# Kernel tuning notes

Measured on AMD Instinct MI355X. Metric: run time of the kernel, lower is better.

The kernel has to match this reference:

```python
import jax, jax.numpy as jnp
import numpy as np

B, N, C, D = 4, 4096, 1024, 32  # batch, tokens, channels, head dim
EPS = 1e-15
PAD_VAL = 1.0


def setup_inputs() -> dict:
    key = jax.random.key(0)
    k1, k2, k3 = jax.random.split(key, 3)
    x = jax.random.normal(k1, (B, N, C), dtype=jnp.float32)
    W_qkv = jax.random.normal(k2, (3 * C, C), dtype=jnp.float32) * 0.02
    W_proj = jax.random.normal(k3, (C, C), dtype=jnp.float32) * 0.02
    b_proj = jnp.zeros((C,), dtype=jnp.float32)
    return {"x": x, "W_qkv": W_qkv, "W_proj": W_proj, "b_proj": b_proj}


def reference(x, W_qkv, W_proj, b_proj):
    Bx, Nx, Cx = x.shape
    h = Cx // D
    # qkv projection (no bias), then split as torch: reshape(B,N,3,C).permute(0,2,3,1)
    qkv = jnp.einsum('bnc,oc->bno', x, W_qkv)            # [B,N,3C]
    qkv = qkv.reshape(Bx, Nx, 3, Cx).transpose(0, 2, 3, 1)  # [B,3,C,N]
    q, k, v = qkv[:, 0], qkv[:, 1], qkv[:, 2]
    q = jax.nn.relu(q.reshape(Bx, h, D, Nx))             # [B,h,D,N]
    k = jax.nn.relu(k.reshape(Bx, h, D, Nx)).transpose(0, 1, 3, 2)  # [B,h,N,D]
    v = v.reshape(Bx, h, D, Nx)                          # [B,h,D,N]
    # pad v with a row of PAD_VAL=1 to carry the normalizer
    v = jnp.concatenate([v, jnp.full((Bx, h, 1, Nx), PAD_VAL, v.dtype)], axis=2)  # [B,h,D+1,N]
    vk = jnp.einsum('bhdn,bhne->bhde', v, k)             # [B,h,D+1,D]
    out = jnp.einsum('bhde,bhen->bhdn', vk, q)           # [B,h,D+1,N]
    out = out[:, :, :-1] / (out[:, :, -1:] + EPS)        # [B,h,D,N]
    out = out.reshape(Bx, Cx, Nx).transpose(0, 2, 1)     # [B,N,C]
    return jnp.einsum('bnc,oc->bno', out, W_proj) + b_proj
```

## Files before the change

kernel.cpp:

```cpp
#include <hip/hip_runtime.h>


using us8   = __attribute__((ext_vector_type(8))) unsigned short;
using us4   = __attribute__((ext_vector_type(4))) unsigned short;
using s8v   = __attribute__((ext_vector_type(8))) short;
using f32x4 = __attribute__((ext_vector_type(4))) float;

__device__ __forceinline__ unsigned short f2bf(float f) {
    union { float f; unsigned int u; } c; c.f = f;
    unsigned int r = c.u + 0x7fffu + ((c.u >> 16) & 1u);
    return (unsigned short)(r >> 16);
}
__device__ __forceinline__ float bf2f(unsigned short u) {
    union { unsigned int u; float f; } c; c.u = ((unsigned int)u) << 16;
    return c.f;
}

__device__ __forceinline__ void async16(const unsigned short* g, unsigned short* l) {
    __builtin_amdgcn_global_load_lds(
        (const __attribute__((address_space(1))) unsigned int*)g,
        (__attribute__((address_space(3))) unsigned int*)l, 16, 0, 0);
}

__global__ __launch_bounds__(256)
void prep(const float* __restrict__ x, const float* __restrict__ wq,
          const float* __restrict__ wp, unsigned short* __restrict__ xb,
          unsigned short* __restrict__ wqb, unsigned short* __restrict__ wpb,
          float* __restrict__ vkws) {
    const int NX = 16777216 / 8, NQ = 3145728 / 8, NP = 1048576 / 8, NZ = 135168 / 8;
    int gid = blockIdx.x * 256 + threadIdx.x;
    const float* in; unsigned short* out; int i;
    if (gid < NX)                    { in = x;  out = xb;  i = gid * 8; }
    else if (gid < NX + NQ)          { in = wq; out = wqb; i = (gid - NX) * 8; }
    else if (gid < NX + NQ + NP)     { in = wp; out = wpb; i = (gid - NX - NQ) * 8; }
    else if (gid < NX + NQ + NP + NZ) {
        int z = (gid - NX - NQ - NP) * 8;
        f32x4 zero = {};
        *(f32x4*)(vkws + z) = zero; *(f32x4*)(vkws + z + 4) = zero;
        return;
    } else return;
    float4 a = *(const float4*)(in + i);
    float4 b = *(const float4*)(in + i + 4);
    us8 o;
    o[0] = f2bf(a.x); o[1] = f2bf(a.y); o[2] = f2bf(a.z); o[3] = f2bf(a.w);
    o[4] = f2bf(b.x); o[5] = f2bf(b.y); o[6] = f2bf(b.z); o[7] = f2bf(b.w);
    *(us8*)(out + i) = o;
}

template <int MODE>
__global__ __launch_bounds__(256)
void gemm_bt(const unsigned short* __restrict__ A,
             const unsigned short* __restrict__ Bt,
             void* __restrict__ C, unsigned short* __restrict__ kvT,
             const float* __restrict__ bias,
             int M, int N, int K) {
    __shared__ unsigned short As0[128 * 32], As1[128 * 32];
    __shared__ unsigned short Bs0[128 * 32], Bs1[128 * 32];

    const int tid  = threadIdx.x;
    const int lane = tid & 63;
    const int wv   = tid >> 6;
    const int wr   = wv >> 1, wc = wv & 1;

    const int MT  = M >> 7;
    const int bpg = MT * 8;
    const int g   = blockIdx.x / bpg;
    const int r   = blockIdx.x % bpg;
    const int tM  = (r >> 3) * 128;
    const int tN  = (g * 8 + (r & 7)) * 128;

    f32x4 acc[4][4] = {};

    const int sseg = ((lane & 3) ^ ((lane >> 3) & 3)) * 8;
    const unsigned short* Ag = A + (size_t)(tM + wv * 32 + (lane >> 2)) * K + sseg;
    const unsigned short* Bg = Bt + (size_t)(tN + wv * 32 + (lane >> 2)) * K + sseg;
    const int wo = wv * 32 * 32;

    const int mrow = lane & 15;
    const int kqx  = (((lane >> 4) ^ ((lane >> 1) & 3))) * 8;

    for (int k0 = 0; k0 < K; k0 += 64) {
        __syncthreads();
        async16(Ag + k0,               &As0[wo]);
        async16(Ag + k0 + 16 * K,      &As0[wo + 16 * 32]);
        async16(Ag + k0 + 32,          &As1[wo]);
        async16(Ag + k0 + 32 + 16 * K, &As1[wo + 16 * 32]);
        async16(Bg + k0,               &Bs0[wo]);
        async16(Bg + k0 + 16 * K,      &Bs0[wo + 16 * 32]);
        async16(Bg + k0 + 32,          &Bs1[wo]);
        async16(Bg + k0 + 32 + 16 * K, &Bs1[wo + 16 * 32]);
        asm volatile("s_waitcnt vmcnt(0)" ::: "memory");
        __syncthreads();
        s8v af[4], bf[4];
#pragma unroll
        for (int mi = 0; mi < 4; ++mi)
            af[mi] = *(const s8v*)&As0[(wr * 64 + mi * 16 + mrow) * 32 + kqx];
#pragma unroll
        for (int ni = 0; ni < 4; ++ni)
            bf[ni] = *(const s8v*)&Bs0[(wc * 64 + ni * 16 + mrow) * 32 + kqx];
#pragma unroll
        for (int mi = 0; mi < 4; ++mi)
#pragma unroll
            for (int ni = 0; ni < 4; ++ni)
                acc[mi][ni] = __builtin_amdgcn_mfma_f32_16x16x32_bf16(
                    af[mi], bf[ni], acc[mi][ni], 0, 0, 0);
#pragma unroll
        for (int mi = 0; mi < 4; ++mi)
            af[mi] = *(const s8v*)&As1[(wr * 64 + mi * 16 + mrow) * 32 + kqx];
#pragma unroll
        for (int ni = 0; ni < 4; ++ni)
            bf[ni] = *(const s8v*)&Bs1[(wc * 64 + ni * 16 + mrow) * 32 + kqx];
#pragma unroll
        for (int mi = 0; mi < 4; ++mi)
#pragma unroll
            for (int ni = 0; ni < 4; ++ni)
                acc[mi][ni] = __builtin_amdgcn_mfma_f32_16x16x32_bf16(
                    af[mi], bf[ni], acc[mi][ni], 0, 0, 0);
    }

    const int crow0 = (lane >> 4) * 4;
    const int ccol  = lane & 15;
    if (MODE == 0 && tN >= 1024) {
        const int b2 = tM >> 12;
        const int nb0 = (tM & 4095) + wr * 64;
#pragma unroll
        for (int mi = 0; mi < 4; ++mi) {
            int nbase = nb0 + mi * 16 + crow0;
#pragma unroll
            for (int ni = 0; ni < 4; ++ni) {
                int col = tN + wc * 64 + ni * 16 + ccol;
                f32x4 v = acc[mi][ni];
                if (col < 2048) {
                    v[0] = fmaxf(v[0], 0.f); v[1] = fmaxf(v[1], 0.f);
                    v[2] = fmaxf(v[2], 0.f); v[3] = fmaxf(v[3], 0.f);
                }
                us4 o;
                o[0] = f2bf(v[0]); o[1] = f2bf(v[1]);
                o[2] = f2bf(v[2]); o[3] = f2bf(v[3]);
                *(us4*)&kvT[((size_t)b2 * 2048 + (col - 1024)) * 4096 + nbase] = o;
            }
        }
    } else {
#pragma unroll
        for (int mi = 0; mi < 4; ++mi)
#pragma unroll
            for (int ni = 0; ni < 4; ++ni) {
                int row = tM + wr * 64 + mi * 16 + crow0;
                int col = tN + wc * 64 + ni * 16 + ccol;
#pragma unroll
                for (int r2 = 0; r2 < 4; ++r2) {
                    float v = acc[mi][ni][r2];
                    if (MODE == 0) {
                        v = fmaxf(v, 0.f);
                        ((unsigned short*)C)[(size_t)(row + r2) * 1024 + col] = f2bf(v);
                    } else {
                        ((float*)C)[(size_t)(row + r2) * N + col] = v + bias[col];
                    }
                }
            }
    }
}

__global__ __launch_bounds__(256)
void lite_vk(const unsigned short* __restrict__ kvT, float* __restrict__ vkws) {
    const int bh = blockIdx.x, ck = blockIdx.y;
    const int b = bh >> 5, h = bh & 31;
    const int S = 136;
    __shared__ unsigned short Ks[32 * S];
    __shared__ unsigned short Vs[32 * S];
    __shared__ float Rs[4][1088];
    const int t = threadIdx.x, lane = t & 63, wv = t >> 6;
    const unsigned short* Kp = kvT + ((size_t)b * 2048 + h * 32) * 4096 + ck * 512;
    const unsigned short* Vp = kvT + ((size_t)b * 2048 + 1024 + h * 32) * 4096 + ck * 512;
    const int sr = t >> 3, ss = (t & 7) * 16;
    f32x4 acc00 = {}, acc01 = {}, acc10 = {}, acc11 = {}, accO0 = {}, accO1 = {};
    s8v ones;
#pragma unroll
    for (int j = 0; j < 8; ++j) ones[j] = (short)0x3F80;
    const int mrow = lane & 15, kq = (lane >> 4) * 8;

    for (int tile = 0; tile < 4; ++tile) {
        int go = tile * 128 + ss;
        us8 k0v = *(const us8*)(Kp + (size_t)sr * 4096 + go);
        us8 k1v = *(const us8*)(Kp + (size_t)sr * 4096 + go + 8);
        us8 v0v = *(const us8*)(Vp + (size_t)sr * 4096 + go);
        us8 v1v = *(const us8*)(Vp + (size_t)sr * 4096 + go + 8);
        __syncthreads();
        *(us8*)&Ks[sr * S + ss]     = k0v;
        *(us8*)&Ks[sr * S + ss + 8] = k1v;
        *(us8*)&Vs[sr * S + ss]     = v0v;
        *(us8*)&Vs[sr * S + ss + 8] = v1v;
        __syncthreads();
        int ko = wv * 32 + kq;
        s8v a0 = *(const s8v*)&Vs[(mrow)      * S + ko];
        s8v a1 = *(const s8v*)&Vs[(16 + mrow) * S + ko];
        s8v b0 = *(const s8v*)&Ks[(mrow)      * S + ko];
        s8v b1 = *(const s8v*)&Ks[(16 + mrow) * S + ko];
        acc00 = __builtin_amdgcn_mfma_f32_16x16x32_bf16(a0, b0, acc00, 0, 0, 0);
        acc01 = __builtin_amdgcn_mfma_f32_16x16x32_bf16(a0, b1, acc01, 0, 0, 0);
        acc10 = __builtin_amdgcn_mfma_f32_16x16x32_bf16(a1, b0, acc10, 0, 0, 0);
        acc11 = __builtin_amdgcn_mfma_f32_16x16x32_bf16(a1, b1, acc11, 0, 0, 0);
        accO0 = __builtin_amdgcn_mfma_f32_16x16x32_bf16(ones, b0, accO0, 0, 0, 0);
        accO1 = __builtin_amdgcn_mfma_f32_16x16x32_bf16(ones, b1, accO1, 0, 0, 0);
    }

    const int ccol = lane & 15, crow = (lane >> 4) * 4;
    float* R = Rs[wv];
#pragma unroll
    for (int r2 = 0; r2 < 4; ++r2) {
        R[(crow + r2) * 32 + ccol]           = acc00[r2];
        R[(crow + r2) * 32 + 16 + ccol]      = acc01[r2];
        R[(16 + crow + r2) * 32 + ccol]      = acc10[r2];
        R[(16 + crow + r2) * 32 + 16 + ccol] = acc11[r2];
    }
    if ((lane >> 4) == 0) {
        R[1024 + ccol]      = accO0[0];
        R[1024 + 16 + ccol] = accO1[0];
    }
    __syncthreads();
    float* vkb = vkws + bh * (33 * 32);
    for (int i = t; i < 1056; i += 256) {
        float s = Rs[0][i] + Rs[1][i] + Rs[2][i] + Rs[3][i];
        atomicAdd(&vkb[i], s);
    }
}

__global__ __launch_bounds__(256)
void lite_apply(const unsigned short* __restrict__ qb,
                const float* __restrict__ vkws,
                unsigned short* __restrict__ yb) {
    const int bh = blockIdx.x, nb = blockIdx.y;
    const int b = bh >> 5, h = bh & 31;
    __shared__ unsigned short vkh[48 * 32];
    __shared__ unsigned short vkl[48 * 32];
    const int t = threadIdx.x;
    for (int i = t; i < 48 * 32; i += 256) {
        float v = (i < 33 * 32) ? vkws[bh * (33 * 32) + i] : 0.f;
        unsigned short hi = f2bf(v);
        vkh[i] = hi;
        vkl[i] = f2bf(v - bf2f(hi));
    }
    __syncthreads();

    const int lane = t & 63, wv = t >> 6;
    const int col = lane & 15, quad = lane >> 4;
    s8v b0h = *(const s8v*)&vkh[(col)      * 32 + quad * 8];
    s8v b0l = *(const s8v*)&vkl[(col)      * 32 + quad * 8];
    s8v b1h = *(const s8v*)&vkh[(16 + col) * 32 + quad * 8];
    s8v b1l = *(const s8v*)&vkl[(16 + col) * 32 + quad * 8];
    s8v b2h = *(const s8v*)&vkh[(32 + col) * 32 + quad * 8];
    s8v b2l = *(const s8v*)&vkl[(32 + col) * 32 + quad * 8];

    const int ntile = nb * 256 + wv * 64;
#pragma unroll
    for (int mi = 0; mi < 4; ++mi) {
        int tok = ntile + mi * 16 + col;
        const unsigned short* qp =
            qb + (size_t)(b * 4096 + tok) * 1024 + h * 32 + quad * 8;
        s8v a = *(const s8v*)qp;
        f32x4 n0 = {}, n1 = {}, dd = {};
        n0 = __builtin_amdgcn_mfma_f32_16x16x32_bf16(b0h, a, n0, 0, 0, 0);
        n0 = __builtin_amdgcn_mfma_f32_16x16x32_bf16(b0l, a, n0, 0, 0, 0);
        n1 = __builtin_amdgcn_mfma_f32_16x16x32_bf16(b1h, a, n1, 0, 0, 0);
        n1 = __builtin_amdgcn_mfma_f32_16x16x32_bf16(b1l, a, n1, 0, 0, 0);
        dd = __builtin_amdgcn_mfma_f32_16x16x32_bf16(b2h, a, dd, 0, 0, 0);
        dd = __builtin_amdgcn_mfma_f32_16x16x32_bf16(b2l, a, dd, 0, 0, 0);
        float den  = __shfl(dd[0], col, 64);
        float rinv = 1.f / (den + 1e-15f);
        us4 o0, o1;
#pragma unroll
        for (int r = 0; r < 4; ++r) {
            o0[r] = f2bf(n0[r] * rinv);
            o1[r] = f2bf(n1[r] * rinv);
        }
        size_t o = (size_t)(b * 4096 + tok) * 1024 + h * 32;
        *(us4*)&yb[o + quad * 4]      = o0;
        *(us4*)&yb[o + 16 + quad * 4] = o1;
    }
}

extern "C" void kernel_launch(void* const* d_in, const int* in_sizes, int n_in,
                              void* d_out, int out_size, void* d_ws, size_t ws_size,
                              hipStream_t stream) {
    const float* x     = (const float*)d_in[0];
    const float* Wqkv  = (const float*)d_in[1];
    const float* Wproj = (const float*)d_in[2];
    const float* bproj = (const float*)d_in[3];
    float* out = (float*)d_out;

    const int M = 16384, Cdim = 1024, O1 = 3072;

    unsigned short* xb     = (unsigned short*)d_ws;
    unsigned short* wqkvb  = xb + (size_t)M * Cdim;
    unsigned short* wprojb = wqkvb + (size_t)O1 * Cdim;
    unsigned short* qb     = wprojb + (size_t)Cdim * Cdim;
    unsigned short* kvT    = qb + (size_t)M * Cdim;
    unsigned short* ybuf   = kvT + (size_t)4 * 2048 * 4096;
    float* vkws            = (float*)(ybuf + (size_t)M * Cdim);

    const int PREP_GROUPS = (16777216 + 3145728 + 1048576 + 135168) / 8;
    prep<<<(PREP_GROUPS + 255) / 256, 256, 0, stream>>>(
        x, Wqkv, Wproj, xb, wqkvb, wprojb, vkws);

    gemm_bt<0><<<(M / 128) * (O1 / 128), 256, 0, stream>>>(
        xb, wqkvb, (void*)qb, kvT, nullptr, M, O1, Cdim);

    lite_vk<<<dim3(128, 8), 256, 0, stream>>>(kvT, vkws);
    lite_apply<<<dim3(128, 16), 256, 0, stream>>>(qb, vkws, ybuf);

    gemm_bt<1><<<(M / 128) * (Cdim / 128), 256, 0, stream>>>(
        ybuf, wprojb, (void*)out, nullptr, bproj, M, Cdim, Cdim);
}
```

Baseline: 359.7 us.

## Fuse vk, apply and projection GEMM into one persistent kernel with grid barriers

Merges the lite_vk, lite_apply and output projection GEMM into a single 512-block persistent kernel. The phases are separated by software grid barriers on an atomic counter that prep zeroes. Each block processes several work units per phase. The aim is to remove two kernel launch gaps and tail effects between small kernels. In exchange it adds spin-wait barrier overhead, relies on all 512 blocks being co-resident (deadlock risk otherwise), and gives the projection GEMM a fixed grid of 512 blocks each doing two tiles.

New measurement: 465.5 us. 1.29x slower.

```diff
diff --git a/kernel.cpp b/kernel.cpp
--- a/kernel.cpp
+++ b/kernel.cpp
@@ -20,6 +20,17 @@
     __builtin_amdgcn_global_load_lds(
         (const __attribute__((address_space(1))) unsigned int*)g,
         (__attribute__((address_space(3))) unsigned int*)l, 16, 0, 0);
+}
+
+__device__ __forceinline__ void grid_barrier(unsigned* cnt, unsigned target) {
+    __syncthreads();
+    if (threadIdx.x == 0) {
+        __threadfence();
+        atomicAdd(cnt, 1u);
+        while (atomicAdd(cnt, 0u) < target) {}
+        __threadfence();
+    }
+    __syncthreads();
 }
 
 __global__ __launch_bounds__(256)
@@ -27,7 +38,8 @@
           const float* __restrict__ wp, unsigned short* __restrict__ xb,
           unsigned short* __restrict__ wqb, unsigned short* __restrict__ wpb,
           float* __restrict__ vkws) {
-    const int NX = 16777216 / 8, NQ = 3145728 / 8, NP = 1048576 / 8, NZ = 135168 / 8;
+    const int NX = 16777216 / 8, NQ = 3145728 / 8, NP = 1048576 / 8;
+    const int NZ = (135168 + 16) / 8;
     int gid = blockIdx.x * 256 + threadIdx.x;
     const float* in; unsigned short* out; int i;
     if (gid < NX)                    { in = x;  out = xb;  i = gid * 8; }
@@ -47,13 +59,11 @@
     *(us8*)(out + i) = o;
 }
 
-template <int MODE>
 __global__ __launch_bounds__(256)
-void gemm_bt(const unsigned short* __restrict__ A,
-             const unsigned short* __restrict__ Bt,
-             void* __restrict__ C, unsigned short* __restrict__ kvT,
-             const float* __restrict__ bias,
-             int M, int N, int K) {
+void gemm_qkv(const unsigned short* __restrict__ A,
+              const unsigned short* __restrict__ Bt,
+              unsigned short* __restrict__ Cq, unsigned short* __restrict__ kvT,
+              int M, int N, int K) {
     __shared__ unsigned short As0[128 * 32], As1[128 * 32];
     __shared__ unsigned short Bs0[128 * 32], Bs1[128 * 32];
 
@@ -120,7 +130,7 @@
 
     const int crow0 = (lane >> 4) * 4;
     const int ccol  = lane & 15;
-    if (MODE == 0 && tN >= 1024) {
+    if (tN >= 1024) {
         const int b2 = tM >> 12;
         const int nb0 = (tM & 4095) + wr * 64;
 #pragma unroll
@@ -149,133 +159,214 @@
                 int col = tN + wc * 64 + ni * 16 + ccol;
 #pragma unroll
                 for (int r2 = 0; r2 < 4; ++r2) {
-                    float v = acc[mi][ni][r2];
-                    if (MODE == 0) {
-                        v = fmaxf(v, 0.f);
-                        ((unsigned short*)C)[(size_t)(row + r2) * 1024 + col] = f2bf(v);
-                    } else {
-                        ((float*)C)[(size_t)(row + r2) * N + col] = v + bias[col];
-                    }
+                    float v = fmaxf(acc[mi][ni][r2], 0.f);
+                    Cq[(size_t)(row + r2) * 1024 + col] = f2bf(v);
                 }
             }
     }
 }
 
-__global__ __launch_bounds__(256)
-void lite_vk(const unsigned short* __restrict__ kvT, float* __restrict__ vkws) {
-    const int bh = blockIdx.x, ck = blockIdx.y;
-    const int b = bh >> 5, h = bh & 31;
-    const int S = 136;
-    __shared__ unsigned short Ks[32 * S];
-    __shared__ unsigned short Vs[32 * S];
-    __shared__ float Rs[4][1088];
-    const int t = threadIdx.x, lane = t & 63, wv = t >> 6;
-    const unsigned short* Kp = kvT + ((size_t)b * 2048 + h * 32) * 4096 + ck * 512;
-    const unsigned short* Vp = kvT + ((size_t)b * 2048 + 1024 + h * 32) * 4096 + ck * 512;
-    const int sr = t >> 3, ss = (t & 7) * 16;
-    f32x4 acc00 = {}, acc01 = {}, acc10 = {}, acc11 = {}, accO0 = {}, accO1 = {};
-    s8v ones;
-#pragma unroll
-    for (int j = 0; j < 8; ++j) ones[j] = (short)0x3F80;
-    const int mrow = lane & 15, kq = (lane >> 4) * 8;
-
-    for (int tile = 0; tile < 4; ++tile) {
-        int go = tile * 128 + ss;
-        us8 k0v = *(const us8*)(Kp + (size_t)sr * 4096 + go);
-        us8 k1v = *(const us8*)(Kp + (size_t)sr * 4096 + go + 8);
-        us8 v0v = *(const us8*)(Vp + (size_t)sr * 4096 + go);
-        us8 v1v = *(const us8*)(Vp + (size_t)sr * 4096 + go + 8);
-        __syncthreads();
-        *(us8*)&Ks[sr * S + ss]     = k0v;
-        *(us8*)&Ks[sr * S + ss + 8] = k1v;
-        *(us8*)&Vs[sr * S + ss]     = v0v;
-        *(us8*)&Vs[sr * S + ss + 8] = v1v;
-        __syncthreads();
-        int ko = wv * 32 + kq;
-        s8v a0 = *(const s8v*)&Vs[(mrow)      * S + ko];
-        s8v a1 = *(const s8v*)&Vs[(16 + mrow) * S + ko];
-        s8v b0 = *(const s8v*)&Ks[(mrow)      * S + ko];
-        s8v b1 = *(const s8v*)&Ks[(16 + mrow) * S + ko];
-        acc00 = __builtin_amdgcn_mfma_f32_16x16x32_bf16(a0, b0, acc00, 0, 0, 0);
-        acc01 = __builtin_amdgcn_mfma_f32_16x16x32_bf16(a0, b1, acc01, 0, 0, 0);
-        acc10 = __builtin_amdgcn_mfma_f32_16x16x32_bf16(a1, b0, acc10, 0, 0, 0);
-        acc11 = __builtin_amdgcn_mfma_f32_16x16x32_bf16(a1, b1, acc11, 0, 0, 0);
-        accO0 = __builtin_amdgcn_mfma_f32_16x16x32_bf16(ones, b0, accO0, 0, 0, 0);
-        accO1 = __builtin_amdgcn_mfma_f32_16x16x32_bf16(ones, b1, accO1, 0, 0, 0);
-    }
-
-    const int ccol = lane & 15, crow = (lane >> 4) * 4;
-    float* R = Rs[wv];
-#pragma unroll
-    for (int r2 = 0; r2 < 4; ++r2) {
-        R[(crow + r2) * 32 + ccol]           = acc00[r2];
-        R[(crow + r2) * 32 + 16 + ccol]      = acc01[r2];
-        R[(16 + crow + r2) * 32 + ccol]      = acc10[r2];
-        R[(16 + crow + r2) * 32 + 16 + ccol] = acc11[r2];
-    }
-    if ((lane >> 4) == 0) {
-        R[1024 + ccol]      = accO0[0];
-        R[1024 + 16 + ccol] = accO1[0];
-    }
-    __syncthreads();
-    float* vkb = vkws + bh * (33 * 32);
-    for (int i = t; i < 1056; i += 256) {
-        float s = Rs[0][i] + Rs[1][i] + Rs[2][i] + Rs[3][i];
-        atomicAdd(&vkb[i], s);
-    }
-}
-
-__global__ __launch_bounds__(256)
-void lite_apply(const unsigned short* __restrict__ qb,
-                const float* __restrict__ vkws,
-                unsigned short* __restrict__ yb) {
-    const int bh = blockIdx.x, nb = blockIdx.y;
-    const int b = bh >> 5, h = bh & 31;
-    __shared__ unsigned short vkh[48 * 32];
-    __shared__ unsigned short vkl[48 * 32];
-    const int t = threadIdx.x;
-    for (int i = t; i < 48 * 32; i += 256) {
-        float v = (i < 33 * 32) ? vkws[bh * (33 * 32) + i] : 0.f;
-        unsigned short hi = f2bf(v);
-        vkh[i] = hi;
-        vkl[i] = f2bf(v - bf2f(hi));
-    }
-    __syncthreads();
-
+__global__ __launch_bounds__(256, 2)
+void attn_tail(const unsigned short* __restrict__ kvT,
+               const unsigned short* __restrict__ qb,
+               unsigned short* __restrict__ ybuf,
+               const unsigned short* __restrict__ wprojb,
+               const float* __restrict__ bias,
+               float* __restrict__ out,
+               float* __restrict__ vkws, unsigned* cnt) {
+    __shared__ char lds[34816];
+    const int blk = blockIdx.x, t = threadIdx.x;
     const int lane = t & 63, wv = t >> 6;
-    const int col = lane & 15, quad = lane >> 4;
-    s8v b0h = *(const s8v*)&vkh[(col)      * 32 + quad * 8];
-    s8v b0l = *(const s8v*)&vkl[(col)      * 32 + quad * 8];
-    s8v b1h = *(const s8v*)&vkh[(16 + col) * 32 + quad * 8];
-    s8v b1l = *(const s8v*)&vkl[(16 + col) * 32 + quad * 8];
-    s8v b2h = *(const s8v*)&vkh[(32 + col) * 32 + quad * 8];
-    s8v b2l = *(const s8v*)&vkl[(32 + col) * 32 + quad * 8];
-
-    const int ntile = nb * 256 + wv * 64;
-#pragma unroll
-    for (int mi = 0; mi < 4; ++mi) {
-        int tok = ntile + mi * 16 + col;
-        const unsigned short* qp =
-            qb + (size_t)(b * 4096 + tok) * 1024 + h * 32 + quad * 8;
-        s8v a = *(const s8v*)qp;
-        f32x4 n0 = {}, n1 = {}, dd = {};
-        n0 = __builtin_amdgcn_mfma_f32_16x16x32_bf16(b0h, a, n0, 0, 0, 0);
-        n0 = __builtin_amdgcn_mfma_f32_16x16x32_bf16(b0l, a, n0, 0, 0, 0);
-        n1 = __builtin_amdgcn_mfma_f32_16x16x32_bf16(b1h, a, n1, 0, 0, 0);
-        n1 = __builtin_amdgcn_mfma_f32_16x16x32_bf16(b1l, a, n1, 0, 0, 0);
-        dd = __builtin_amdgcn_mfma_f32_16x16x32_bf16(b2h, a, dd, 0, 0, 0);
-        dd = __builtin_amdgcn_mfma_f32_16x16x32_bf16(b2l, a, dd, 0, 0, 0);
-        float den  = __shfl(dd[0], col, 64);
-        float rinv = 1.f / (den + 1e-15f);
-        us4 o0, o1;
-#pragma unroll
-        for (int r = 0; r < 4; ++r) {
-            o0[r] = f2bf(n0[r] * rinv);
-            o1[r] = f2bf(n1[r] * rinv);
+
+    {
+        const int S = 136;
+        unsigned short* Ks = (unsigned short*)lds;
+        unsigned short* Vs = (unsigned short*)(lds + 8704);
+        float* Rsb = (float*)(lds + 17408);
+        const int sr = t >> 3, ss = (t & 7) * 16;
+        const int mrow = lane & 15, kq = (lane >> 4) * 8;
+        s8v ones;
+#pragma unroll
+        for (int j2 = 0; j2 < 8; ++j2) ones[j2] = (short)0x3F80;
+
+        for (int j = 0; j < 2; ++j) {
+            const int u = blk * 2 + j;
+            const int bh = u >> 3, ck = u & 7;
+            const int b = bh >> 5, h = bh & 31;
+            const unsigned short* Kp = kvT + ((size_t)b * 2048 + h * 32) * 4096 + ck * 512;
+            const unsigned short* Vp = kvT + ((size_t)b * 2048 + 1024 + h * 32) * 4096 + ck * 512;
+            f32x4 a00 = {}, a01 = {}, a10 = {}, a11 = {}, aO0 = {}, aO1 = {};
+            for (int tile = 0; tile < 4; ++tile) {
+                int go = tile * 128 + ss;
+                us8 k0v = *(const us8*)(Kp + (size_t)sr * 4096 + go);
+                us8 k1v = *(const us8*)(Kp + (size_t)sr * 4096 + go + 8);
+                us8 v0v = *(const us8*)(Vp + (size_t)sr * 4096 + go);
+                us8 v1v = *(const us8*)(Vp + (size_t)sr * 4096 + go + 8);
+                __syncthreads();
+                *(us8*)&Ks[sr * S + ss]     = k0v;
+                *(us8*)&Ks[sr * S + ss + 8] = k1v;
+                *(us8*)&Vs[sr * S + ss]     = v0v;
+                *(us8*)&Vs[sr * S + ss + 8] = v1v;
+                __syncthreads();
+                int ko = wv * 32 + kq;
+                s8v a0 = *(const s8v*)&Vs[(mrow)      * S + ko];
+                s8v a1 = *(const s8v*)&Vs[(16 + mrow) * S + ko];
+                s8v b0 = *(const s8v*)&Ks[(mrow)      * S + ko];
+                s8v b1 = *(const s8v*)&Ks[(16 + mrow) * S + ko];
+                a00 = __builtin_amdgcn_mfma_f32_16x16x32_bf16(a0, b0, a00, 0, 0, 0);
+                a01 = __builtin_amdgcn_mfma_f32_16x16x32_bf16(a0, b1, a01, 0, 0, 0);
+                a10 = __builtin_amdgcn_mfma_f32_16x16x32_bf16(a1, b0, a10, 0, 0, 0);
+                a11 = __builtin_amdgcn_mfma_f32_16x16x32_bf16(a1, b1, a11, 0, 0, 0);
+                aO0 = __builtin_amdgcn_mfma_f32_16x16x32_bf16(ones, b0, aO0, 0, 0, 0);
+                aO1 = __builtin_amdgcn_mfma_f32_16x16x32_bf16(ones, b1, aO1, 0, 0, 0);
+            }
+            const int ccol = lane & 15, crow = (lane >> 4) * 4;
+            float* R = Rsb + wv * 1088;
+#pragma unroll
+            for (int r2 = 0; r2 < 4; ++r2) {
+                R[(crow + r2) * 32 + ccol]           = a00[r2];
+                R[(crow + r2) * 32 + 16 + ccol]      = a01[r2];
+                R[(16 + crow + r2) * 32 + ccol]      = a10[r2];
+                R[(16 + crow + r2) * 32 + 16 + ccol] = a11[r2];
+            }
+            if ((lane >> 4) == 0) {
+                R[1024 + ccol]      = aO0[0];
+                R[1024 + 16 + ccol] = aO1[0];
+            }
+            __syncthreads();
+            float* vkb = vkws + bh * (33 * 32);
+            for (int i = t; i < 1056; i += 256) {
+                float s = Rsb[i] + Rsb[1088 + i] + Rsb[2176 + i] + Rsb[3264 + i];
+                atomicAdd(&vkb[i], s);
+            }
+            __syncthreads();
         }
-        size_t o = (size_t)(b * 4096 + tok) * 1024 + h * 32;
-        *(us4*)&yb[o + quad * 4]      = o0;
-        *(us4*)&yb[o + 16 + quad * 4] = o1;
+    }
+    grid_barrier(cnt, 512);
+
+    {
+        unsigned short* vkh = (unsigned short*)lds;
+        unsigned short* vkl = (unsigned short*)(lds + 3072);
+        const int col = lane & 15, quad = lane >> 4;
+        for (int j = 0; j < 4; ++j) {
+            const int u = blk * 4 + j;
+            const int bh = u >> 4, nb = u & 15;
+            const int b = bh >> 5, h = bh & 31;
+            for (int i = t; i < 48 * 32; i += 256) {
+                float v = (i < 33 * 32) ? vkws[bh * (33 * 32) + i] : 0.f;
+                unsigned short hi = f2bf(v);
+                vkh[i] = hi;
+                vkl[i] = f2bf(v - bf2f(hi));
+            }
+            __syncthreads();
+            s8v b0h = *(const s8v*)&vkh[(col)      * 32 + quad * 8];
+            s8v b0l = *(const s8v*)&vkl[(col)      * 32 + quad * 8];
+            s8v b1h = *(const s8v*)&vkh[(16 + col) * 32 + quad * 8];
+            s8v b1l = *(const s8v*)&vkl[(16 + col) * 32 + quad * 8];
+            s8v b2h = *(const s8v*)&vkh[(32 + col) * 32 + quad * 8];
+            s8v b2l = *(const s8v*)&vkl[(32 + col) * 32 + quad * 8];
+            const int ntile = nb * 256 + wv * 64;
+#pragma unroll
+            for (int mi = 0; mi < 4; ++mi) {
+                int tok = ntile + mi * 16 + col;
+                const unsigned short* qp =
+                    qb + (size_t)(b * 4096 + tok) * 1024 + h * 32 + quad * 8;
+                s8v a = *(const s8v*)qp;
+                f32x4 n0 = {}, n1 = {}, dd = {};
+                n0 = __builtin_amdgcn_mfma_f32_16x16x32_bf16(b0h, a, n0, 0, 0, 0);
+                n0 = __builtin_amdgcn_mfma_f32_16x16x32_bf16(b0l, a, n0, 0, 0, 0);
+                n1 = __builtin_amdgcn_mfma_f32_16x16x32_bf16(b1h, a, n1, 0, 0, 0);
+                n1 = __builtin_amdgcn_mfma_f32_16x16x32_bf16(b1l, a, n1, 0, 0, 0);
+                dd = __builtin_amdgcn_mfma_f32_16x16x32_bf16(b2h, a, dd, 0, 0, 0);
+                dd = __builtin_amdgcn_mfma_f32_16x16x32_bf16(b2l, a, dd, 0, 0, 0);
+                float den  = __shfl(dd[0], col, 64);
+                float rinv = 1.f / (den + 1e-15f);
+                us4 o0, o1;
+#pragma unroll
+                for (int r2 = 0; r2 < 4; ++r2) {
+                    o0[r2] = f2bf(n0[r2] * rinv);
+                    o1[r2] = f2bf(n1[r2] * rinv);
+                }
+                size_t o = (size_t)(b * 4096 + tok) * 1024 + h * 32;
+                *(us4*)&ybuf[o + quad * 4]      = o0;
+                *(us4*)&ybuf[o + 16 + quad * 4] = o1;
+            }
+            __syncthreads();
+        }
+    }
+    grid_barrier(cnt, 1024);
+
+    {
+        unsigned short* As0 = (unsigned short*)lds;
+        unsigned short* As1 = (unsigned short*)(lds + 8192);
+        unsigned short* Bs0 = (unsigned short*)(lds + 16384);
+        unsigned short* Bs1 = (unsigned short*)(lds + 24576);
+        const int K = 1024;
+        const int wr = wv >> 1, wc = wv & 1;
+        const int sseg = ((lane & 3) ^ ((lane >> 3) & 3)) * 8;
+        const int mrow = lane & 15;
+        const int kqx  = (((lane >> 4) ^ ((lane >> 1) & 3))) * 8;
+        const int wo = wv * 32 * 32;
+
+        for (int j = 0; j < 2; ++j) {
+            const int u = blk * 2 + j;
+            const int tM = (u >> 3) * 128;
+            const int tN = (u & 7) * 128;
+            f32x4 acc[4][4] = {};
+            const unsigned short* Ag = ybuf + (size_t)(tM + wv * 32 + (lane >> 2)) * K + sseg;
+            const unsigned short* Bg = wprojb + (size_t)(tN + wv * 32 + (lane >> 2)) * K + sseg;
+            for (int k0 = 0; k0 < K; k0 += 64) {
+                __syncthreads();
+                async16(Ag + k0,               &As0[wo]);
+                async16(Ag + k0 + 16 * K,      &As0[wo + 16 * 32]);
+                async16(Ag + k0 + 32,          &As1[wo]);
+                async16(Ag + k0 + 32 + 16 * K, &As1[wo + 16 * 32]);
+                async16(Bg + k0,               &Bs0[wo]);
+                async16(Bg + k0 + 16 * K,      &Bs0[wo + 16 * 32]);
+                async16(Bg + k0 + 32,          &Bs1[wo]);
+                async16(Bg + k0 + 32 + 16 * K, &Bs1[wo + 16 * 32]);
+                asm volatile("s_waitcnt vmcnt(0)" ::: "memory");
+                __syncthreads();
+                s8v af[4], bf[4];
+#pragma unroll
+                for (int mi = 0; mi < 4; ++mi)
+                    af[mi] = *(const s8v*)&As0[(wr * 64 + mi * 16 + mrow) * 32 + kqx];
+#pragma unroll
+                for (int ni = 0; ni < 4; ++ni)
+                    bf[ni] = *(const s8v*)&Bs0[(wc * 64 + ni * 16 + mrow) * 32 + kqx];
+#pragma unroll
+                for (int mi = 0; mi < 4; ++mi)
+#pragma unroll
+                    for (int ni = 0; ni < 4; ++ni)
+                        acc[mi][ni] = __builtin_amdgcn_mfma_f32_16x16x32_bf16(
+                            af[mi], bf[ni], acc[mi][ni], 0, 0, 0);
+#pragma unroll
+                for (int mi = 0; mi < 4; ++mi)
+                    af[mi] = *(const s8v*)&As1[(wr * 64 + mi * 16 + mrow) * 32 + kqx];
+#pragma unroll
+                for (int ni = 0; ni < 4; ++ni)
+                    bf[ni] = *(const s8v*)&Bs1[(wc * 64 + ni * 16 + mrow) * 32 + kqx];
+#pragma unroll
+                for (int mi = 0; mi < 4; ++mi)
+#pragma unroll
+                    for (int ni = 0; ni < 4; ++ni)
+                        acc[mi][ni] = __builtin_amdgcn_mfma_f32_16x16x32_bf16(
+                            af[mi], bf[ni], acc[mi][ni], 0, 0, 0);
+            }
+            const int crow0 = (lane >> 4) * 4;
+            const int ccol  = lane & 15;
+#pragma unroll
+            for (int mi = 0; mi < 4; ++mi)
+#pragma unroll
+                for (int ni = 0; ni < 4; ++ni) {
+                    int row = tM + wr * 64 + mi * 16 + crow0;
+                    int col = tN + wc * 64 + ni * 16 + ccol;
+#pragma unroll
+                    for (int r2 = 0; r2 < 4; ++r2)
+                        out[(size_t)(row + r2) * 1024 + col] = acc[mi][ni][r2] + bias[col];
+                }
+            __syncthreads();
+        }
     }
 }
 
@@ -297,17 +388,15 @@
     unsigned short* kvT    = qb + (size_t)M * Cdim;
     unsigned short* ybuf   = kvT + (size_t)4 * 2048 * 4096;
     float* vkws            = (float*)(ybuf + (size_t)M * Cdim);
-
-    const int PREP_GROUPS = (16777216 + 3145728 + 1048576 + 135168) / 8;
+    unsigned* cnt          = (unsigned*)(vkws + 135168);
+
+    const int PREP_GROUPS = (16777216 + 3145728 + 1048576 + 135168 + 16) / 8;
     prep<<<(PREP_GROUPS + 255) / 256, 256, 0, stream>>>(
         x, Wqkv, Wproj, xb, wqkvb, wprojb, vkws);
 
-    gemm_bt<0><<<(M / 128) * (O1 / 128), 256, 0, stream>>>(
-        xb, wqkvb, (void*)qb, kvT, nullptr, M, O1, Cdim);
-
-    lite_vk<<<dim3(128, 8), 256, 0, stream>>>(kvT, vkws);
-    lite_apply<<<dim3(128, 16), 256, 0, stream>>>(qb, vkws, ybuf);
-
-    gemm_bt<1><<<(M / 128) * (Cdim / 128), 256, 0, stream>>>(
-        ybuf, wprojb, (void*)out, nullptr, bproj, M, Cdim, Cdim);
-}
+    gemm_qkv<<<(M / 128) * (O1 / 128), 256, 0, stream>>>(
+        xb, wqkvb, qb, kvT, M, O1, Cdim);
+
+    attn_tail<<<512, 256, 0, stream>>>(
+        kvT, qb, ybuf, wprojb, bproj, out, vkws, cnt);
+}
```
